# Optimization experiments

Hardware: AMD Instinct MI355X
Metric: run time of the kernel (lower is better)

## Reference

```python
import jax, jax.numpy as jnp
import numpy as np

B, S, Z = 64, 512, 256
HID, L = 1024, 1024


def _lstm_cell(x, h, c, Wih, Whh, bih, bhh):
    # torch LSTMCell gate order: i, f, g, o
    gates = x @ Wih.T + bih + h @ Whh.T + bhh  # [B, 4L]
    i, f, g, o = jnp.split(gates, 4, axis=-1)
    i, f, o = jax.nn.sigmoid(i), jax.nn.sigmoid(f), jax.nn.sigmoid(o)
    g = jnp.tanh(g)
    c_new = f * c + i * g
    h_new = o * jnp.tanh(c_new)
    return h_new, c_new


def setup_inputs() -> dict:
    key = jax.random.key(0)
    ks = jax.random.split(key, 16)
    sc = 0.05
    return {
        "z": jax.random.normal(ks[0], (B, S, Z), jnp.float32),
        "prev_gen0": jax.random.uniform(ks[1], (B, Z), jnp.float32),
        "h1": jnp.zeros((B, L), jnp.float32),
        "c1": jnp.zeros((B, L), jnp.float32),
        "h2": jnp.zeros((B, L), jnp.float32),
        "c2": jnp.zeros((B, L), jnp.float32),
        "W1": jax.random.normal(ks[2], (HID, 2 * Z), jnp.float32) * sc,
        "b1": jnp.zeros((HID,), jnp.float32),
        "Wih1": jax.random.normal(ks[3], (4 * L, HID), jnp.float32) * sc,
        "Whh1": jax.random.normal(ks[4], (4 * L, L), jnp.float32) * sc,
        "bih1": jnp.zeros((4 * L,), jnp.float32),
        "bhh1": jnp.zeros((4 * L,), jnp.float32),
        "Wih2": jax.random.normal(ks[5], (4 * L, L), jnp.float32) * sc,
        "Whh2": jax.random.normal(ks[6], (4 * L, L), jnp.float32) * sc,
        "bih2": jnp.zeros((4 * L,), jnp.float32),
        "bhh2": jnp.zeros((4 * L,), jnp.float32),
        "W2": jax.random.normal(ks[7], (Z, L), jnp.float32) * sc,
        "b2": jnp.zeros((Z,), jnp.float32),
    }


def reference(z, prev_gen0, h1, c1, h2, c2, W1, b1, Wih1, Whh1, bih1, bhh1,
              Wih2, Whh2, bih2, bhh2, W2, b2):
    z_t = jnp.transpose(z, (1, 0, 2))  # [S, B, Z]

    def step(carry, z_step):
        prev_gen, h1, c1, h2, c2 = carry
        concat_in = jnp.concatenate([z_step, prev_gen], axis=-1)  # [B, 2Z]
        out = jax.nn.relu(concat_in @ W1.T + b1)                  # [B, HID]
        h1, c1 = _lstm_cell(out, h1, c1, Wih1, Whh1, bih1, bhh1)
        # dropout disabled (inference / deterministic reference)
        h2, c2 = _lstm_cell(h1, h2, c2, Wih2, Whh2, bih2, bhh2)
        prev_gen = h2 @ W2.T + b2                                 # [B, Z]
        return (prev_gen, h1, c1, h2, c2), prev_gen

    (_, h1, c1, h2, c2), feats = jax.lax.scan(
        step, (prev_gen0, h1, c1, h2, c2), z_t)
    gen_feats = jnp.transpose(feats, (1, 0, 2))  # [B, S, Z]
    return gen_feats, (h1, c1), (h2, c2)
```

## Files before the change

### kernel.cpp

```cpp
#include <hip/hip_runtime.h>

#define NB 64
#define NS 512
#define NZ 256
#define NH 1024
#define NWG 256
#define NT 512

typedef _Float16 f16;
typedef unsigned long long u64;
typedef __attribute__((ext_vector_type(8))) _Float16 half8;
typedef __attribute__((ext_vector_type(4))) float f32x4;

#define WS_BAR  0
#define WS_B1P  4096
#define WS_PG0  8192
#define WS_WF   40960
#define WS_ACT  2138112
#define SLOTF 65536
#define REQ_BYTES (2138112ull + 3ull * 513ull * 131072ull)

__device__ __forceinline__ float sigf(float x) { return 1.f / (1.f + __expf(-x)); }
__device__ __forceinline__ float tanhfast(float x) { return 2.f / (1.f + __expf(-2.f * x)) - 1.f; }

__device__ __forceinline__ f32x4 MF(half8 a, half8 b, f32x4 c) {
  return __builtin_amdgcn_mfma_f32_16x16x32_f16(a, b, c, 0, 0, 0);
}

__device__ __forceinline__ u64 ald8(const f16* p) {
  return __hip_atomic_load((const u64*)p, __ATOMIC_RELAXED, __HIP_MEMORY_SCOPE_AGENT);
}
template <bool CACHED>
__device__ __forceinline__ half8 ldc(const f16* base, int kk, int kg, int R) {
  int ch = 8 * kk + 2 * kg;
  union { u64 u[2]; half8 h; } x;
  if (CACHED) {
    x.u[0] = *(const u64*)(base + ((size_t)(ch * 64 + R) * 4));
    x.u[1] = *(const u64*)(base + ((size_t)((ch + 1) * 64 + R) * 4));
  } else {
    x.u[0] = ald8(base + ((size_t)(ch * 64 + R) * 4));
    x.u[1] = ald8(base + ((size_t)((ch + 1) * 64 + R) * 4));
  }
  return x.h;
}
__device__ __forceinline__ void ast4f(float* p, float v) {
  __hip_atomic_store((unsigned*)(void*)p, __float_as_uint(v), __ATOMIC_RELAXED, __HIP_MEMORY_SCOPE_AGENT);
}
__device__ __forceinline__ void store_act(f16* base, int w, int m, float hvf) {
  f16 hv = (f16)hvf;
  unsigned short hb; __builtin_memcpy(&hb, &hv, 2);
  int l = threadIdx.x & 63;
  int c_ = l & 15;
  int v1 = __shfl((int)hb, c_ + 16);
  int v2 = __shfl((int)hb, c_ + 32);
  int v3 = __shfl((int)hb, c_ + 48);
  if (l < 16) {
    int R = 16 * m + c_;
    u64 val = (u64)hb | ((u64)(unsigned short)v1 << 16)
            | ((u64)(unsigned short)v2 << 32) | ((u64)(unsigned short)v3 << 48);
    __hip_atomic_store((u64*)(base + ((size_t)(w * 64 + R) * 4)), val,
                       __ATOMIC_RELAXED, __HIP_MEMORY_SCOPE_AGENT);
  }
}
template <bool CACHED>
__device__ __forceinline__ void gemm_half(const f16* base, const char* brow, int bofs,
                                          int kh, int kg, int R, f32x4& a0, f32x4& a1) {
  #pragma unroll 8
  for (int i = 0; i < 16; ++i) {
    int kk = kh * 16 + i;
    half8 a = ldc<CACHED>(base, kk, kg, R);
    half8 b = *(const half8*)(brow + bofs + kk * 64);
    if (i & 1) a1 = MF(a, b, a1); else a0 = MF(a, b, a0);
  }
}

__device__ __forceinline__ void bar_arrive(char* bar, int w) {
  asm volatile("s_waitcnt vmcnt(0)" ::: "memory");
  __syncthreads();
  if (threadIdx.x == 0) {
    unsigned* cnt = (unsigned*)(bar + (size_t)(w >> 4) * 128);
    __hip_atomic_fetch_add(cnt, 1u, __ATOMIC_RELAXED, __HIP_MEMORY_SCOPE_AGENT);
  }
}
__device__ __forceinline__ void bar_wait(char* bar, unsigned e) {
  if (threadIdx.x < 64) {
    unsigned* cnt = (unsigned*)(bar + (size_t)(threadIdx.x & 15) * 128);
    unsigned tgt = e << 4;
    while (true) {
      unsigned v = __hip_atomic_load(cnt, __ATOMIC_RELAXED, __HIP_MEMORY_SCOPE_AGENT);
      if (__all((int)(v >= tgt))) break;
      __builtin_amdgcn_s_sleep(8);
    }
    asm volatile("" ::: "memory");
  }
  __syncthreads();
}

#define L_W0   0
#define L_W2   10304
#define L_W1   12368
#define L_WP2  78160
#define L_W1P  143952
#define L_X    146064
#define L_X2   150160
#define L_X3   154256
#define LDS_BYTES 154512

__global__ void init_state(const float* __restrict__ h1, const float* __restrict__ h2,
                           const float* __restrict__ pg0, const float* __restrict__ W1,
                           const float* __restrict__ b1, const float* __restrict__ b2,
                           char* __restrict__ ws, size_t h2off) {
  int i = blockIdx.x * blockDim.x + threadIdx.x;
  int R = i & 63;
  int U = i >> 6;
  f16* H1s0 = (f16*)(ws + WS_ACT);
  f16* H2s0 = (f16*)(ws + WS_ACT) + h2off;
  int pidx = ((U >> 2) * 64 + R) * 4 + (U & 3);
  H1s0[pidx] = (f16)h1[(size_t)R * NH + U];
  H2s0[pidx] = (f16)h2[(size_t)R * NH + U];
  if (i < 16384) {
    int u = i >> 6, r2 = i & 63;
    ((f16*)(ws + WS_PG0))[((u >> 2) * 64 + r2) * 4 + (u & 3)] = (f16)pg0[(size_t)r2 * NZ + u];
  }
  if (i < NH) {
    float acc = b1[i];
    const float* wp = W1 + (size_t)i * (2 * NZ) + NZ;
    for (int mm = 0; mm < NZ; ++mm) acc = fmaf(wp[mm], b2[mm], acc);
    ((float*)(ws + WS_B1P))[i] = acc;
  }
  if (i < 1024) ((unsigned*)(ws + WS_BAR))[i] = 0u;
}

__global__ void prep_wfused(const float* __restrict__ W1, const float* __restrict__ W2,
                            char* __restrict__ ws) {
  int u = blockIdx.x >> 2;
  int j = ((blockIdx.x & 3) << 8) + threadIdx.x;
  const float* wp = W1 + (size_t)u * (2 * NZ) + NZ;
  float acc = 0.f;
  for (int mm = 0; mm < NZ; ++mm) acc = fmaf(wp[mm], W2[(size_t)mm * NH + j], acc);
  ((f16*)(ws + WS_WF))[(size_t)u * NH + j] = (f16)acc;
}

template <bool CACHED>
__global__ __launch_bounds__(NT, 1) void gen_persistent(
    const float* __restrict__ z,
    const float* __restrict__ W1, const float* __restrict__ b1,
    const float* __restrict__ Wih1, const float* __restrict__ Whh1,
    const float* __restrict__ bih1, const float* __restrict__ bhh1,
    const float* __restrict__ Wih2, const float* __restrict__ Whh2,
    const float* __restrict__ bih2, const float* __restrict__ bhh2,
    const float* __restrict__ W2, const float* __restrict__ b2,
    const float* __restrict__ c1in, const float* __restrict__ c2in,
    float* __restrict__ dout, char* __restrict__ ws, size_t h2off, size_t outoff)
{
  extern __shared__ char smem[];
  const int w = blockIdx.x;
  const int tid = threadIdx.x;
  const int w8 = tid >> 6;
  const int m = w8 & 3;
  const int kh = w8 >> 2;
  const int l = tid & 63;
  const int c = l & 15;
  const int kg = l >> 4;

  f16* H1base = (f16*)(ws + WS_ACT);
  f16* H2base = H1base + h2off;
  f16* Outbase = H1base + outoff;
  const f16* Wf = (const f16*)(ws + WS_WF);
  const f16* Pg0p = (const f16*)(ws + WS_PG0);
  const float* b1p = (const float*)(ws + WS_B1P);
  char* bar = ws + WS_BAR;

  for (int i = 0; i < 16; ++i) {
    int gi = i >> 2, uu = 4 * w + (i & 3);
    const float* s1i = Wih1 + (size_t)(gi * NH + uu) * NH;
    const float* s1h = Whh1 + (size_t)(gi * NH + uu) * NH;
    const float* s2i = Wih2 + (size_t)(gi * NH + uu) * NH;
    const float* s2h = Whh2 + (size_t)(gi * NH + uu) * NH;
    f16* d1 = (f16*)(smem + L_W1 + i * 4112);
    f16* d2 = (f16*)(smem + L_WP2 + i * 4112);
    for (int k = tid; k < NH; k += NT) {
      d1[k] = (f16)s1i[k]; d1[NH + k] = (f16)s1h[k];
      d2[k] = (f16)s2i[k]; d2[NH + k] = (f16)s2h[k];
    }
  }
  for (int i = 0; i < 4; ++i) {
    int uu = 4 * w + i;
    f16* d0 = (f16*)(smem + L_W0 + i * 2576);
    if (tid < 256) d0[tid] = (f16)W1[(size_t)uu * (2 * NZ) + tid];
    for (int k = tid; k < NH; k += NT) d0[NZ + k] = Wf[(size_t)uu * NH + k];
    f16* dp = (f16*)(smem + L_W1P + i * 528);
    if (tid < 256) dp[tid] = (f16)W1[(size_t)uu * (2 * NZ) + NZ + tid];
  }
  {
    f16* dw2 = (f16*)(smem + L_W2);
    for (int k = tid; k < NH; k += NT) dw2[k] = (f16)W2[(size_t)w * NH + k];
  }
  __syncthreads();

  const int R = 16 * m + c;
  const int U = 4 * w + kg;
  const float b0fused = b1p[U];
  const float b0plain = b1[U];
  const float bi1 = bih1[U] + bhh1[U];
  const float bf1 = bih1[NH + U] + bhh1[NH + U];
  const float bg1 = bih1[2 * NH + U] + bhh1[2 * NH + U];
  const float bo1 = bih1[3 * NH + U] + bhh1[3 * NH + U];
  const float bi2 = bih2[U] + bhh2[U];
  const float bf2 = bih2[NH + U] + bhh2[NH + U];
  const float bg2 = bih2[2 * NH + U] + bhh2[2 * NH + U];
  const float bo2 = bih2[3 * NH + U] + bhh2[3 * NH + U];
  const float b2w = b2[w];

  float c1reg = c1in[(size_t)R * NH + U];
  float c2reg = c2in[(size_t)R * NH + U];
  float h1last = 0.f, h2last = 0.f;

  float* scr  = (float*)(smem + L_X) + m * 256;
  float* scr3 = (float*)(smem + L_X3) + m * 16;
  const char* brow0 = smem + L_W0 + (c & 3) * 2576 + kg * 16;
  const char* brow2 = smem + L_W2 + kg * 16;
  const char* brow1 = smem + L_W1 + c * 4112 + kg * 16;
  const char* browp2 = smem + L_WP2 + c * 4112 + kg * 16;
  const char* browp0 = smem + L_W1P + (c & 3) * 528 + kg * 16;
  const float* zlane = z + (size_t)R * NS * NZ + kg * 8;

  for (int t = 0; t < NS; ++t) {
    const int sp = CACHED ? t : (t & 1);
    const int sn = CACHED ? (t + 1) : ((t + 1) & 1);
    const f16* h2prev = H2base + (size_t)sp * SLOTF;
    const f16* h1prev = H1base + (size_t)sp * SLOTF;
    f16* h1new = H1base + (size_t)sn * SLOTF;
    f16* h2new = H2base + (size_t)sn * SLOTF;
    f16* outb = Outbase + (size_t)sn * SLOTF;
    const unsigned eb = 3u * (unsigned)t;

    f32x4 ao0 = {0.f,0.f,0.f,0.f}, ao1 = ao0, ap0 = ao0, ap1 = ao0;
    if (t == 0) {
      if (kh == 0) {
        #pragma unroll
        for (int kk = 0; kk < 8; ++kk) {
          f32x4 f0 = *(const f32x4*)(zlane + kk * 32);
          f32x4 f1 = *(const f32x4*)(zlane + kk * 32 + 4);
          half8 a;
          a[0]=(f16)f0[0]; a[1]=(f16)f0[1]; a[2]=(f16)f0[2]; a[3]=(f16)f0[3];
          a[4]=(f16)f1[0]; a[5]=(f16)f1[1]; a[6]=(f16)f1[2]; a[7]=(f16)f1[3];
          half8 b = *(const half8*)(brow0 + kk * 64);
          if (kk & 1) ao1 = MF(a, b, ao1); else ao0 = MF(a, b, ao0);
        }
      } else {
        #pragma unroll
        for (int kk = 0; kk < 8; ++kk) {
          half8 a = ldc<true>(Pg0p, kk, kg, R);
          half8 b = *(const half8*)(browp0 + kk * 64);
          if (kk & 1) ao1 = MF(a, b, ao1); else ao0 = MF(a, b, ao0);
        }
      }
      bar_wait(bar, eb);
    } else {
      const float* zt = zlane + (size_t)t * NZ;
      #pragma unroll
      for (int i = 0; i < 4; ++i) {
        int kk = kh * 4 + i;
        f32x4 f0 = *(const f32x4*)(zt + kk * 32);
        f32x4 f1 = *(const f32x4*)(zt + kk * 32 + 4);
        half8 a;
        a[0]=(f16)f0[0]; a[1]=(f16)f0[1]; a[2]=(f16)f0[2]; a[3]=(f16)f0[3];
        a[4]=(f16)f1[0]; a[5]=(f16)f1[1]; a[6]=(f16)f1[2]; a[7]=(f16)f1[3];
        half8 b = *(const half8*)(brow0 + kk * 64);
        if (i & 1) ao1 = MF(a, b, ao1); else ao0 = MF(a, b, ao0);
      }
      bar_wait(bar, eb);
      #pragma unroll 8
      for (int i = 0; i < 16; ++i) {
        int kk = kh * 16 + i;
        half8 a = ldc<CACHED>(h2prev, kk, kg, R);
        half8 bwf = *(const half8*)(brow0 + 512 + kk * 64);
        half8 bw2 = *(const half8*)(brow2 + kk * 64);
        if (i & 1) { ao1 = MF(a, bwf, ao1); ap1 = MF(a, bw2, ap1); }
        else       { ao0 = MF(a, bwf, ao0); ap0 = MF(a, bw2, ap0); }
      }
    }
    f32x4 Dp;
    {
      float* s2 = (float*)(smem + L_X2) + m * 256;
      f32x4 D = ao0 + ao1;
      Dp = ap0 + ap1;
      if (kh == 0) {
        if (c < 4) {
          #pragma unroll
          for (int v = 0; v < 4; ++v) s2[c * 16 + kg * 4 + v] = D[v];
        }
        if (c == 0 && t > 0) {
          #pragma unroll
          for (int v = 0; v < 4; ++v) scr3[kg * 4 + v] = Dp[v];
        }
      }
      __syncthreads();
      if (kh == 1) {
        if (c < 4) {
          #pragma unroll
          for (int v = 0; v < 4; ++v) scr[c * 16 + kg * 4 + v] = D[v] + s2[c * 16 + kg * 4 + v];
        }
        float pre = scr[kg * 16 + c] + ((t == 0) ? b0plain : b0fused);
        store_act(outb, w, m, fmaxf(pre, 0.f));
      }
    }
    bar_arrive(bar, w);
    if (kh == 1 && t > 0 && c == 0) {
      #pragma unroll
      for (int v = 0; v < 4; ++v) {
        int Rp = 16 * m + kg * 4 + v;
        ast4f(&dout[((size_t)Rp * NS + (t - 1)) * NZ + w], Dp[v] + scr3[kg * 4 + v] + b2w);
      }
    }

    {
      f32x4 g0 = {0.f,0.f,0.f,0.f}, g1 = g0;
      gemm_half<CACHED>(h1prev, brow1, 2048, kh, kg, R, g0, g1);
      bar_wait(bar, eb + 1);
      gemm_half<CACHED>(outb, brow1, 0, kh, kg, R, g0, g1);
      float* s2 = (float*)(smem + L_X2) + m * 256;
      f32x4 D = g0 + g1;
      if (kh == 0) {
        #pragma unroll
        for (int v = 0; v < 4; ++v) s2[c * 16 + kg * 4 + v] = D[v];
      }
      __syncthreads();
      if (kh == 1) {
        #pragma unroll
        for (int v = 0; v < 4; ++v) scr[c * 16 + kg * 4 + v] = D[v] + s2[c * 16 + kg * 4 + v];
        float ai = scr[kg * 16 + c];
        float af = scr[(4 + kg) * 16 + c];
        float ag = scr[(8 + kg) * 16 + c];
        float aoo = scr[(12 + kg) * 16 + c];
        float iv = sigf(ai + bi1), fv = sigf(af + bf1);
        float gv = tanhfast(ag + bg1), ov = sigf(aoo + bo1);
        float cn = fmaf(fv, c1reg, iv * gv);
        c1reg = cn;
        float hv = ov * tanhfast(cn);
        h1last = hv;
        store_act(h1new, w, m, hv);
      }
    }
    bar_arrive(bar, w);

    {
      f32x4 q0 = {0.f,0.f,0.f,0.f}, q1 = q0;
      gemm_half<CACHED>(h2prev, browp2, 2048, kh, kg, R, q0, q1);
      bar_wait(bar, eb + 2);
      gemm_half<CACHED>(h1new, browp2, 0, kh, kg, R, q0, q1);
      float* s2 = (float*)(smem + L_X2) + m * 256;
      f32x4 D = q0 + q1;
      if (kh == 0) {
        #pragma unroll
        for (int v = 0; v < 4; ++v) s2[c * 16 + kg * 4 + v] = D[v];
      }
      __syncthreads();
      if (kh == 1) {
        #pragma unroll
        for (int v = 0; v < 4; ++v) scr[c * 16 + kg * 4 + v] = D[v] + s2[c * 16 + kg * 4 + v];
        float ai = scr[kg * 16 + c];
        float af = scr[(4 + kg) * 16 + c];
        float ag = scr[(8 + kg) * 16 + c];
        float aoo = scr[(12 + kg) * 16 + c];
        float iv = sigf(ai + bi2), fv = sigf(af + bf2);
        float gv = tanhfast(ag + bg2), ov = sigf(aoo + bo2);
        float cn = fmaf(fv, c2reg, iv * gv);
        c2reg = cn;
        float hv = ov * tanhfast(cn);
        h2last = hv;
        store_act(h2new, w, m, hv);
      }
    }
    bar_arrive(bar, w);
  }

  bar_wait(bar, 3u * NS);
  {
    const f16* h2fin = H2base + (size_t)(CACHED ? NS : 0) * SLOTF;
    f32x4 t0 = {0.f,0.f,0.f,0.f}, t1 = t0;
    gemm_half<CACHED>(h2fin, brow2, 0, kh, kg, R, t0, t1);
    f32x4 Dp2 = t0 + t1;
    if (kh == 0 && c == 0) {
      #pragma unroll
      for (int v = 0; v < 4; ++v) scr3[kg * 4 + v] = Dp2[v];
    }
    __syncthreads();
    if (kh == 1 && c == 0) {
      #pragma unroll
      for (int v = 0; v < 4; ++v) {
        int Rp = 16 * m + kg * 4 + v;
        dout[((size_t)Rp * NS + (NS - 1)) * NZ + w] = Dp2[v] + scr3[kg * 4 + v] + b2w;
      }
    }
  }

  if (kh == 1) {
    float* o = dout + (size_t)NB * NS * NZ;
    o[(size_t)R * NH + U] = h1last;
    o[(size_t)NB * NH + (size_t)R * NH + U] = c1reg;
    o[2 * (size_t)NB * NH + (size_t)R * NH + U] = h2last;
    o[3 * (size_t)NB * NH + (size_t)R * NH + U] = c2reg;
  }
}

extern "C" void kernel_launch(void* const* d_in, const int* in_sizes, int n_in,
                              void* d_out, int out_size, void* d_ws, size_t ws_size,
                              hipStream_t stream) {
  const float* z    = (const float*)d_in[0];
  const float* pg0  = (const float*)d_in[1];
  const float* h1   = (const float*)d_in[2];
  const float* c1   = (const float*)d_in[3];
  const float* h2   = (const float*)d_in[4];
  const float* c2   = (const float*)d_in[5];
  const float* W1   = (const float*)d_in[6];
  const float* b1   = (const float*)d_in[7];
  const float* Wih1 = (const float*)d_in[8];
  const float* Whh1 = (const float*)d_in[9];
  const float* bih1 = (const float*)d_in[10];
  const float* bhh1 = (const float*)d_in[11];
  const float* Wih2 = (const float*)d_in[12];
  const float* Whh2 = (const float*)d_in[13];
  const float* bih2 = (const float*)d_in[14];
  const float* bhh2 = (const float*)d_in[15];
  const float* W2   = (const float*)d_in[16];
  const float* b2   = (const float*)d_in[17];
  char* ws = (char*)d_ws;
  float* out = (float*)d_out;

  const bool big = ws_size >= (size_t)REQ_BYTES;
  const size_t h2off  = big ? (size_t)513 * SLOTF : (size_t)2 * SLOTF;
  const size_t outoff = big ? (size_t)1026 * SLOTF : (size_t)4 * SLOTF;

  hipLaunchKernelGGL(init_state, dim3(256), dim3(256), 0, stream,
                     h1, h2, pg0, W1, b1, b2, ws, h2off);
  hipLaunchKernelGGL(prep_wfused, dim3(4096), dim3(256), 0, stream, W1, W2, ws);
  if (big) {
    hipLaunchKernelGGL((gen_persistent<true>), dim3(NWG), dim3(NT), LDS_BYTES, stream,
                       z, W1, b1, Wih1, Whh1, bih1, bhh1, Wih2, Whh2, bih2, bhh2, W2, b2,
                       c1, c2, out, ws, h2off, outoff);
  } else {
    hipLaunchKernelGGL((gen_persistent<false>), dim3(NWG), dim3(NT), LDS_BYTES, stream,
                       z, W1, b1, Wih1, Whh1, bih1, bhh1, Wih2, Whh2, bih2, bhh2, W2, b2,
                       c1, c2, out, ws, h2off, outoff);
  }
}
```

Before: 8.861 ms.

## Precompute z projection in a separate kernel and replace block barriers with per-wave arrivals

Adds an xz_prep kernel that computes the z half of the first linear layer for all timesteps ahead of time with MFMA, storing fp16 results in workspace so the persistent loop only adds a scalar per step. It also removes the __syncthreads-based barrier arrive/wait, letting each kh==1 wave arrive through an LDS counter, with the fourth arrival bumping the global counter. The scratch buffers are double-buffered so consecutive phases do not race. The trade-offs are extra workspace and a prep launch, finer-grained synchronization that is harder to get right, and a z path used only when the workspace is large enough.

```diff
diff --git a/kernel.cpp b/kernel.cpp
--- a/kernel.cpp
+++ b/kernel.cpp
@@ -18,7 +18,9 @@
 #define WS_WF   40960
 #define WS_ACT  2138112
 #define SLOTF 65536
-#define REQ_BYTES (2138112ull + 3ull * 513ull * 131072ull)
+#define REQ1 (2138112ull + 3ull * 513ull * 131072ull)
+#define XZOFF_B REQ1
+#define REQ2 (XZOFF_B + 512ull * 1024ull * 64ull * 2ull)
 
 __device__ __forceinline__ float sigf(float x) { return 1.f / (1.f + __expf(-x)); }
 __device__ __forceinline__ float tanhfast(float x) { return 2.f / (1.f + __expf(-2.f * x)) - 1.f; }
@@ -45,6 +47,13 @@
 }
 __device__ __forceinline__ void ast4f(float* p, float v) {
   __hip_atomic_store((unsigned*)(void*)p, __float_as_uint(v), __ATOMIC_RELAXED, __HIP_MEMORY_SCOPE_AGENT);
+}
+__device__ __forceinline__ u64 pack4h(f32x4 d) {
+  f16 a = (f16)d[0], b = (f16)d[1], c = (f16)d[2], e = (f16)d[3];
+  unsigned short ua, ub, uc, ue;
+  __builtin_memcpy(&ua, &a, 2); __builtin_memcpy(&ub, &b, 2);
+  __builtin_memcpy(&uc, &c, 2); __builtin_memcpy(&ue, &e, 2);
+  return (u64)ua | ((u64)ub << 16) | ((u64)uc << 32) | ((u64)ue << 48);
 }
 __device__ __forceinline__ void store_act(f16* base, int w, int m, float hvf) {
   f16 hv = (f16)hvf;
@@ -74,26 +83,24 @@
   }
 }
 
-__device__ __forceinline__ void bar_arrive(char* bar, int w) {
+__device__ __forceinline__ void bar_wait(char* bar, unsigned e) {
+  const unsigned* cnt = (const unsigned*)(bar + (size_t)(threadIdx.x & 15) * 128);
+  const unsigned tgt = e << 4;
+  for (;;) {
+    unsigned v = __hip_atomic_load(cnt, __ATOMIC_RELAXED, __HIP_MEMORY_SCOPE_AGENT);
+    if (__all((int)(v >= tgt))) break;
+    __builtin_amdgcn_s_sleep(4);
+  }
+  asm volatile("" ::: "memory");
+}
+__device__ __forceinline__ void arrive_kh1(char* bar, int w, unsigned* ctrE) {
   asm volatile("s_waitcnt vmcnt(0)" ::: "memory");
-  __syncthreads();
-  if (threadIdx.x == 0) {
-    unsigned* cnt = (unsigned*)(bar + (size_t)(w >> 4) * 128);
-    __hip_atomic_fetch_add(cnt, 1u, __ATOMIC_RELAXED, __HIP_MEMORY_SCOPE_AGENT);
-  }
-}
-__device__ __forceinline__ void bar_wait(char* bar, unsigned e) {
-  if (threadIdx.x < 64) {
-    unsigned* cnt = (unsigned*)(bar + (size_t)(threadIdx.x & 15) * 128);
-    unsigned tgt = e << 4;
-    while (true) {
-      unsigned v = __hip_atomic_load(cnt, __ATOMIC_RELAXED, __HIP_MEMORY_SCOPE_AGENT);
-      if (__all((int)(v >= tgt))) break;
-      __builtin_amdgcn_s_sleep(8);
-    }
-    asm volatile("" ::: "memory");
-  }
-  __syncthreads();
+  if ((threadIdx.x & 63) == 0) {
+    unsigned prev = __hip_atomic_fetch_add(ctrE, 1u, __ATOMIC_ACQ_REL, __HIP_MEMORY_SCOPE_WORKGROUP);
+    if ((prev & 3u) == 3u)
+      __hip_atomic_fetch_add((unsigned*)(bar + (size_t)(w >> 4) * 128), 1u,
+                             __ATOMIC_RELAXED, __HIP_MEMORY_SCOPE_AGENT);
+  }
 }
 
 #define L_W0   0
@@ -103,8 +110,9 @@
 #define L_W1P  143952
 #define L_X    146064
 #define L_X2   150160
-#define L_X3   154256
-#define LDS_BYTES 154512
+#define L_X3   158352
+#define L_CTR  158608
+#define LDS_BYTES 158640
 
 __global__ void init_state(const float* __restrict__ h1, const float* __restrict__ h2,
                            const float* __restrict__ pg0, const float* __restrict__ W1,
@@ -141,7 +149,47 @@
   ((f16*)(ws + WS_WF))[(size_t)u * NH + j] = (f16)acc;
 }
 
-template <bool CACHED>
+__global__ __launch_bounds__(512, 1) void xz_prep(const float* __restrict__ z,
+                                                  const float* __restrict__ W1,
+                                                  f16* __restrict__ xz) {
+  __shared__ f16 Wz[64 * 256];
+  const int ug = (int)blockIdx.x >> 5;
+  const int tq = (int)blockIdx.x & 31;
+  const int tid = threadIdx.x;
+  const int base_u = ug * 64;
+  for (int i = tid; i < 64 * 256; i += 512) {
+    int uu = i >> 8, k = i & 255;
+    Wz[i] = (f16)W1[(size_t)(base_u + uu) * (2 * NZ) + k];
+  }
+  __syncthreads();
+  const int m = (tid >> 6) & 3;
+  const int uh = tid >> 8;
+  const int l = tid & 63;
+  const int c = l & 15;
+  const int kg = l >> 4;
+  const int R = 16 * m + c;
+  for (int tt = 0; tt < 16; ++tt) {
+    int t = tq * 16 + tt;
+    const float* zt = z + (size_t)R * NS * NZ + (size_t)t * NZ + kg * 8;
+    f32x4 a0 = {0.f, 0.f, 0.f, 0.f}, a1 = a0;
+    #pragma unroll
+    for (int kk = 0; kk < 8; ++kk) {
+      f32x4 f0 = *(const f32x4*)(zt + kk * 32);
+      f32x4 f1 = *(const f32x4*)(zt + kk * 32 + 4);
+      half8 a;
+      a[0]=(f16)f0[0]; a[1]=(f16)f0[1]; a[2]=(f16)f0[2]; a[3]=(f16)f0[3];
+      a[4]=(f16)f1[0]; a[5]=(f16)f1[1]; a[6]=(f16)f1[2]; a[7]=(f16)f1[3];
+      half8 b0 = *(const half8*)(Wz + (uh * 32 + c) * 256 + kk * 32 + kg * 8);
+      half8 b1 = *(const half8*)(Wz + (uh * 32 + 16 + c) * 256 + kk * 32 + kg * 8);
+      a0 = MF(a, b0, a0);
+      a1 = MF(a, b1, a1);
+    }
+    *(u64*)(xz + (((size_t)t * NH + base_u + uh * 32 + c) * 64 + 16 * m + kg * 4)) = pack4h(a0);
+    *(u64*)(xz + (((size_t)t * NH + base_u + uh * 32 + 16 + c) * 64 + 16 * m + kg * 4)) = pack4h(a1);
+  }
+}
+
+template <bool CACHED, bool XZPRE>
 __global__ __launch_bounds__(NT, 1) void gen_persistent(
     const float* __restrict__ z,
     const float* __restrict__ W1, const float* __restrict__ b1,
@@ -151,7 +199,8 @@
     const float* __restrict__ bih2, const float* __restrict__ bhh2,
     const float* __restrict__ W2, const float* __restrict__ b2,
     const float* __restrict__ c1in, const float* __restrict__ c2in,
-    float* __restrict__ dout, char* __restrict__ ws, size_t h2off, size_t outoff)
+    float* __restrict__ dout, char* __restrict__ ws,
+    size_t h2off, size_t outoff, const f16* __restrict__ xz)
 {
   extern __shared__ char smem[];
   const int w = blockIdx.x;
@@ -170,6 +219,7 @@
   const f16* Pg0p = (const f16*)(ws + WS_PG0);
   const float* b1p = (const float*)(ws + WS_B1P);
   char* bar = ws + WS_BAR;
+  unsigned* ctrE = (unsigned*)(smem + L_CTR);
 
   for (int i = 0; i < 16; ++i) {
     int gi = i >> 2, uu = 4 * w + (i & 3);
@@ -196,6 +246,7 @@
     f16* dw2 = (f16*)(smem + L_W2);
     for (int k = tid; k < NH; k += NT) dw2[k] = (f16)W2[(size_t)w * NH + k];
   }
+  if (tid == 0) *ctrE = 0u;
   __syncthreads();
 
   const int R = 16 * m + c;
@@ -225,6 +276,8 @@
   const char* browp0 = smem + L_W1P + (c & 3) * 528 + kg * 16;
   const float* zlane = z + (size_t)R * NS * NZ + kg * 8;
 
+  int sb = 0;
+
   for (int t = 0; t < NS; ++t) {
     const int sp = CACHED ? t : (t & 1);
     const int sn = CACHED ? (t + 1) : ((t + 1) & 1);
@@ -235,9 +288,11 @@
     f16* outb = Outbase + (size_t)sn * SLOTF;
     const unsigned eb = 3u * (unsigned)t;
 
+    float xzv = 0.f;
+    if (XZPRE && kh == 1) xzv = (float)xz[((size_t)t * NH + U) * 64 + R];
     f32x4 ao0 = {0.f,0.f,0.f,0.f}, ao1 = ao0, ap0 = ao0, ap1 = ao0;
     if (t == 0) {
-      if (kh == 0) {
+      if (!XZPRE && kh == 0) {
         #pragma unroll
         for (int kk = 0; kk < 8; ++kk) {
           f32x4 f0 = *(const f32x4*)(zlane + kk * 32);
@@ -248,7 +303,8 @@
           half8 b = *(const half8*)(brow0 + kk * 64);
           if (kk & 1) ao1 = MF(a, b, ao1); else ao0 = MF(a, b, ao0);
         }
-      } else {
+      }
+      if (kh == 1) {
         #pragma unroll
         for (int kk = 0; kk < 8; ++kk) {
           half8 a = ldc<true>(Pg0p, kk, kg, R);
@@ -258,17 +314,19 @@
       }
       bar_wait(bar, eb);
     } else {
-      const float* zt = zlane + (size_t)t * NZ;
-      #pragma unroll
-      for (int i = 0; i < 4; ++i) {
-        int kk = kh * 4 + i;
-        f32x4 f0 = *(const f32x4*)(zt + kk * 32);
-        f32x4 f1 = *(const f32x4*)(zt + kk * 32 + 4);
-        half8 a;
-        a[0]=(f16)f0[0]; a[1]=(f16)f0[1]; a[2]=(f16)f0[2]; a[3]=(f16)f0[3];
-        a[4]=(f16)f1[0]; a[5]=(f16)f1[1]; a[6]=(f16)f1[2]; a[7]=(f16)f1[3];
-        half8 b = *(const half8*)(brow0 + kk * 64);
-        if (i & 1) ao1 = MF(a, b, ao1); else ao0 = MF(a, b, ao0);
+      if (!XZPRE) {
+        const float* zt = zlane + (size_t)t * NZ;
+        #pragma unroll
+        for (int i = 0; i < 4; ++i) {
+          int kk = kh * 4 + i;
+          f32x4 f0 = *(const f32x4*)(zt + kk * 32);
+          f32x4 f1 = *(const f32x4*)(zt + kk * 32 + 4);
+          half8 a;
+          a[0]=(f16)f0[0]; a[1]=(f16)f0[1]; a[2]=(f16)f0[2]; a[3]=(f16)f0[3];
+          a[4]=(f16)f1[0]; a[5]=(f16)f1[1]; a[6]=(f16)f1[2]; a[7]=(f16)f1[3];
+          half8 b = *(const half8*)(brow0 + kk * 64);
+          if (i & 1) ao1 = MF(a, b, ao1); else ao0 = MF(a, b, ao0);
+        }
       }
       bar_wait(bar, eb);
       #pragma unroll 8
@@ -283,7 +341,7 @@
     }
     f32x4 Dp;
     {
-      float* s2 = (float*)(smem + L_X2) + m * 256;
+      float* s2 = (float*)(smem + L_X2 + (sb << 12)) + m * 256;
       f32x4 D = ao0 + ao1;
       Dp = ap0 + ap1;
       if (kh == 0) {
@@ -302,25 +360,26 @@
           #pragma unroll
           for (int v = 0; v < 4; ++v) scr[c * 16 + kg * 4 + v] = D[v] + s2[c * 16 + kg * 4 + v];
         }
-        float pre = scr[kg * 16 + c] + ((t == 0) ? b0plain : b0fused);
+        float pre = scr[kg * 16 + c] + xzv + ((t == 0) ? b0plain : b0fused);
         store_act(outb, w, m, fmaxf(pre, 0.f));
-      }
-    }
-    bar_arrive(bar, w);
-    if (kh == 1 && t > 0 && c == 0) {
-      #pragma unroll
-      for (int v = 0; v < 4; ++v) {
-        int Rp = 16 * m + kg * 4 + v;
-        ast4f(&dout[((size_t)Rp * NS + (t - 1)) * NZ + w], Dp[v] + scr3[kg * 4 + v] + b2w);
-      }
-    }
+        arrive_kh1(bar, w, ctrE);
+        if (t > 0 && c == 0) {
+          #pragma unroll
+          for (int v = 0; v < 4; ++v) {
+            int Rp = 16 * m + kg * 4 + v;
+            ast4f(&dout[((size_t)Rp * NS + (t - 1)) * NZ + w], Dp[v] + scr3[kg * 4 + v] + b2w);
+          }
+        }
+      }
+    }
+    sb ^= 1;
 
     {
       f32x4 g0 = {0.f,0.f,0.f,0.f}, g1 = g0;
       gemm_half<CACHED>(h1prev, brow1, 2048, kh, kg, R, g0, g1);
       bar_wait(bar, eb + 1);
       gemm_half<CACHED>(outb, brow1, 0, kh, kg, R, g0, g1);
-      float* s2 = (float*)(smem + L_X2) + m * 256;
+      float* s2 = (float*)(smem + L_X2 + (sb << 12)) + m * 256;
       f32x4 D = g0 + g1;
       if (kh == 0) {
         #pragma unroll
@@ -341,16 +400,17 @@
         float hv = ov * tanhfast(cn);
         h1last = hv;
         store_act(h1new, w, m, hv);
-      }
-    }
-    bar_arrive(bar, w);
+        arrive_kh1(bar, w, ctrE);
+      }
+    }
+    sb ^= 1;
 
     {
       f32x4 q0 = {0.f,0.f,0.f,0.f}, q1 = q0;
       gemm_half<CACHED>(h2prev, browp2, 2048, kh, kg, R, q0, q1);
       bar_wait(bar, eb + 2);
       gemm_half<CACHED>(h1new, browp2, 0, kh, kg, R, q0, q1);
-      float* s2 = (float*)(smem + L_X2) + m * 256;
+      float* s2 = (float*)(smem + L_X2 + (sb << 12)) + m * 256;
       f32x4 D = q0 + q1;
       if (kh == 0) {
         #pragma unroll
@@ -371,9 +431,10 @@
         float hv = ov * tanhfast(cn);
         h2last = hv;
         store_act(h2new, w, m, hv);
-      }
-    }
-    bar_arrive(bar, w);
+        arrive_kh1(bar, w, ctrE);
+      }
+    }
+    sb ^= 1;
   }
 
   bar_wait(bar, 3u * NS);
@@ -429,20 +490,27 @@
   char* ws = (char*)d_ws;
   float* out = (float*)d_out;
 
-  const bool big = ws_size >= (size_t)REQ_BYTES;
+  const bool big = ws_size >= (size_t)REQ1;
+  const bool xzm = ws_size >= (size_t)REQ2;
   const size_t h2off  = big ? (size_t)513 * SLOTF : (size_t)2 * SLOTF;
   const size_t outoff = big ? (size_t)1026 * SLOTF : (size_t)4 * SLOTF;
+  f16* xzp = (f16*)(ws + XZOFF_B);
 
   hipLaunchKernelGGL(init_state, dim3(256), dim3(256), 0, stream,
                      h1, h2, pg0, W1, b1, b2, ws, h2off);
   hipLaunchKernelGGL(prep_wfused, dim3(4096), dim3(256), 0, stream, W1, W2, ws);
-  if (big) {
-    hipLaunchKernelGGL((gen_persistent<true>), dim3(NWG), dim3(NT), LDS_BYTES, stream,
+  if (xzm) {
+    hipLaunchKernelGGL(xz_prep, dim3(512), dim3(512), 0, stream, z, W1, xzp);
+    hipLaunchKernelGGL((gen_persistent<true, true>), dim3(NWG), dim3(NT), LDS_BYTES, stream,
                        z, W1, b1, Wih1, Whh1, bih1, bhh1, Wih2, Whh2, bih2, bhh2, W2, b2,
-                       c1, c2, out, ws, h2off, outoff);
+                       c1, c2, out, ws, h2off, outoff, xzp);
+  } else if (big) {
+    hipLaunchKernelGGL((gen_persistent<true, false>), dim3(NWG), dim3(NT), LDS_BYTES, stream,
+                       z, W1, b1, Wih1, Whh1, bih1, bhh1, Wih2, Whh2, bih2, bhh2, W2, b2,
+                       c1, c2, out, ws, h2off, outoff, xzp);
   } else {
-    hipLaunchKernelGGL((gen_persistent<false>), dim3(NWG), dim3(NT), LDS_BYTES, stream,
+    hipLaunchKernelGGL((gen_persistent<false, false>), dim3(NWG), dim3(NT), LDS_BYTES, stream,
                        z, W1, b1, Wih1, Whh1, bih1, bhh1, Wih2, Whh2, bih2, bhh2, W2, b2,
-                       c1, c2, out, ws, h2off, outoff);
-  }
-}
+                       c1, c2, out, ws, h2off, outoff, xzp);
+  }
+}
```

Result: slower. 12.92 ms (+45.8%).
